# Performance work log

Measured on AMD Instinct MI355X. Metric: run time of the kernel, lower is better.

Reference implementation:

```python
import jax, jax.numpy as jnp
import numpy as np


def setup_inputs() -> dict:
    key = jax.random.key(0)
    k_u, k_wl, k_b, k_c = jax.random.split(key, 4)
    B_, T, D, N = 4, 4096, 1024, 256
    u = jax.random.normal(k_u, (B_, T, D), dtype=jnp.float32)
    # torch init: W_lambda.weight zeros, bias 2.0; B, C xavier_uniform gain=0.5.
    # Use small random weights for W_lambda too so the path is exercised.
    Wl = jax.random.normal(k_wl, (N, D), dtype=jnp.float32) * 0.02
    bl = jnp.full((N,), 2.0, dtype=jnp.float32)
    xav_b = 0.5 * np.sqrt(6.0 / (D + N))
    Wb = jax.random.uniform(k_b, (N, D), dtype=jnp.float32, minval=-xav_b, maxval=xav_b)
    xav_c = 0.5 * np.sqrt(6.0 / (N + D))
    Wc = jax.random.uniform(k_c, (D, N), dtype=jnp.float32, minval=-xav_c, maxval=xav_c)
    Dp = jnp.zeros((D,), dtype=jnp.float32)
    return {"u": u, "Wl": Wl, "bl": bl, "Wb": Wb, "Wc": Wc, "Dp": Dp}


def reference(u, Wl, bl, Wb, Wc, Dp):
    # u: (B, T, D). Precompute per-step gates and inputs with batched GEMMs,
    # then run the diagonal linear recurrence with lax.scan over time.
    lam = jax.nn.sigmoid(jnp.einsum('btd,nd->btn', u, Wl) + bl)  # (B, T, N)
    Bu = jnp.einsum('btd,nd->btn', u, Wb)                         # (B, T, N)

    def step(h, inp):
        lam_t, bu_t = inp            # each (B, N)
        h = lam_t * h + bu_t
        return h, h

    h0 = jnp.zeros((u.shape[0], Wl.shape[0]), dtype=u.dtype)
    # scan over time: move T to leading axis
    _, H = jax.lax.scan(step, h0, (jnp.swapaxes(lam, 0, 1), jnp.swapaxes(Bu, 0, 1)))
    H = jnp.swapaxes(H, 0, 1)        # (B, T, N)
    y = jnp.einsum('btn,dn->btd', H, Wc) + u * Dp
    return y
```

## Files before the change

kernel.cpp:

```cpp
#include <hip/hip_runtime.h>


typedef __bf16 bf16_t;
typedef __attribute__((ext_vector_type(8))) __bf16 bf16x8;
typedef __attribute__((ext_vector_type(4))) __bf16 bf16x4;
typedef __attribute__((ext_vector_type(4))) float f32x4;

#define B_  4
#define T_  4096
#define D_  1024
#define N_  256
#define BT  (B_ * T_)
#define NCHUNK 64
#define CHLEN  (T_ / NCHUNK)

#define GLOAD_LDS16(g, l) __builtin_amdgcn_global_load_lds(              \
    (__attribute__((address_space(1))) void*)(g),                        \
    (__attribute__((address_space(3))) void*)(l), 16, 0, 0)

__global__ void cvt_f32_bf16(const float* __restrict__ in,
                             bf16_t* __restrict__ out, int n4) {
  int i = blockIdx.x * 256 + threadIdx.x;
  if (i >= n4) return;
  float4 v = ((const float4*)in)[i];
  bf16x4 o = {(__bf16)v.x, (__bf16)v.y, (__bf16)v.z, (__bf16)v.w};
  ((bf16x4*)out)[i] = o;
}

__global__ void cvt_wcomb(const float* __restrict__ Wl,
                          const float* __restrict__ Wb,
                          bf16_t* __restrict__ out) {
  int i = blockIdx.x * 256 + threadIdx.x;
  int e = i * 4;
  int j = e >> 10;
  int d = e & 1023;
  const float* src = (j < 256) ? (Wl + (size_t)j * D_ + d)
                               : (Wb + (size_t)(j - 256) * D_ + d);
  float4 v = *(const float4*)src;
  bf16x4 o = {(__bf16)v.x, (__bf16)v.y, (__bf16)v.z, (__bf16)v.w};
  ((bf16x4*)out)[i] = o;
}

__device__ __forceinline__ void mfma_tile(const bf16_t* bufA, const bf16_t* bufB,
                                          int wr, int wc, int r16, int kq,
                                          f32x4 (&acc)[4][4]) {
#pragma unroll
  for (int kk = 0; kk < 2; ++kk) {
    bf16x8 af[4], bfr[4];
#pragma unroll
    for (int m = 0; m < 4; ++m)
      af[m] = *(const bf16x8*)&bufA[(wr * 64 + m * 16 + r16) * 64 + kk * 32 + kq * 8];
#pragma unroll
    for (int n = 0; n < 4; ++n)
      bfr[n] = *(const bf16x8*)&bufB[(wc * 64 + n * 16 + r16) * 64 + kk * 32 + kq * 8];
#pragma unroll
    for (int m = 0; m < 4; ++m)
#pragma unroll
      for (int n = 0; n < 4; ++n)
        acc[m][n] = __builtin_amdgcn_mfma_f32_16x16x32_bf16(af[m], bfr[n], acc[m][n], 0, 0, 0);
  }
}

__global__ __launch_bounds__(256)
void gemm1_kernel(const float* __restrict__ A, const bf16_t* __restrict__ Bm,
                  float* __restrict__ C, const float* __restrict__ bl) {
  __shared__ bf16_t lA[2][128 * 64];
  __shared__ bf16_t lB[2][128 * 64];
  const int wid  = threadIdx.x >> 6;
  const int lane = threadIdx.x & 63;
  const int work = (blockIdx.x & 7) * 64 + (blockIdx.x >> 3);
  const int brow = work >> 2;
  const int bcol = work & 3;
  const int r16 = lane & 15;
  const int kq  = lane >> 4;
  const int wr = wid >> 1, wc = wid & 1;

  f32x4 acc[4][4] = {};

  const int ar = lane >> 4;
  const int ac = (lane & 15) * 4;
  const float* gA = A + (size_t)(brow * 128 + wid * 32 + ar) * D_ + ac;
  bf16_t* lAw[2] = {&lA[0][(wid * 32 + ar) * 64 + ac],
                    &lA[1][(wid * 32 + ar) * 64 + ac]};

  const bf16_t* gB = Bm + (size_t)(bcol * 128 + wid * 8 + (lane >> 3)) * D_ + (lane & 7) * 8;

  {
    float4 va[8];
#pragma unroll
    for (int i = 0; i < 8; ++i)
      va[i] = *(const float4*)(gA + (size_t)(i * 4) * D_);
#pragma unroll
    for (int i = 0; i < 4; ++i)
      GLOAD_LDS16(gB + (size_t)(i * 32) * D_, &lB[0][(wid * 8 + i * 32) * 64]);
#pragma unroll
    for (int i = 0; i < 8; ++i) {
      bf16x4 o = {(__bf16)va[i].x, (__bf16)va[i].y,
                  (__bf16)va[i].z, (__bf16)va[i].w};
      *(bf16x4*)(lAw[0] + i * 4 * 64) = o;
    }
    __syncthreads();
  }

  int cur = 0;
#pragma unroll 1
  for (int k0 = 0; k0 < D_ - 64; k0 += 64) {
    float4 va[8];
#pragma unroll
    for (int i = 0; i < 8; ++i)
      va[i] = *(const float4*)(gA + (size_t)(i * 4) * D_ + k0 + 64);
#pragma unroll
    for (int i = 0; i < 4; ++i)
      GLOAD_LDS16(gB + (size_t)(i * 32) * D_ + k0 + 64,
                  &lB[cur ^ 1][(wid * 8 + i * 32) * 64]);
    mfma_tile(lA[cur], lB[cur], wr, wc, r16, kq, acc);
#pragma unroll
    for (int i = 0; i < 8; ++i) {
      bf16x4 o = {(__bf16)va[i].x, (__bf16)va[i].y,
                  (__bf16)va[i].z, (__bf16)va[i].w};
      *(bf16x4*)(lAw[cur ^ 1] + i * 4 * 64) = o;
    }
    __syncthreads();
    cur ^= 1;
  }
  mfma_tile(lA[cur], lB[cur], wr, wc, r16, kq, acc);

#pragma unroll
  for (int m = 0; m < 4; ++m) {
#pragma unroll
    for (int n = 0; n < 4; ++n) {
      int row0 = brow * 128 + wr * 64 + m * 16 + kq * 4;
      int col  = bcol * 128 + wc * 64 + n * 16 + r16;
#pragma unroll
      for (int j = 0; j < 4; ++j) {
        float v = acc[m][n][j];
        int row = row0 + j;
        if (col < 256) v = 1.0f / (1.0f + __expf(-(v + bl[col])));
        C[(size_t)row * 512 + col] = v;
      }
    }
  }
}

__global__ __launch_bounds__(256)
void gemm2_kernel(const bf16_t* __restrict__ A, const bf16_t* __restrict__ Bm,
                  float* __restrict__ C,
                  const float* __restrict__ u, const float* __restrict__ Dp) {
  __shared__ bf16_t lA[2][128 * 64];
  __shared__ bf16_t lB[2][128 * 64];
  const int wid  = threadIdx.x >> 6;
  const int lane = threadIdx.x & 63;
  const int brow = blockIdx.x;
  const int bcol = blockIdx.y;
  const int r16 = lane & 15;
  const int kq  = lane >> 4;
  const int wr = wid >> 1, wc = wid & 1;

  f32x4 acc[4][4] = {};

  const bf16_t* gA = A + (size_t)(brow * 128 + wid * 8 + (lane >> 3)) * N_ + (lane & 7) * 8;
  const bf16_t* gB = Bm + (size_t)(bcol * 128 + wid * 8 + (lane >> 3)) * N_ + (lane & 7) * 8;

  {
#pragma unroll
    for (int i = 0; i < 4; ++i) {
      GLOAD_LDS16(gA + (size_t)(i * 32) * N_, &lA[0][(wid * 8 + i * 32) * 64]);
      GLOAD_LDS16(gB + (size_t)(i * 32) * N_, &lB[0][(wid * 8 + i * 32) * 64]);
    }
    __syncthreads();
  }
  int cur = 0;
#pragma unroll 1
  for (int k0 = 0; k0 < N_ - 64; k0 += 64) {
#pragma unroll
    for (int i = 0; i < 4; ++i) {
      GLOAD_LDS16(gA + (size_t)(i * 32) * N_ + k0 + 64,
                  &lA[cur ^ 1][(wid * 8 + i * 32) * 64]);
      GLOAD_LDS16(gB + (size_t)(i * 32) * N_ + k0 + 64,
                  &lB[cur ^ 1][(wid * 8 + i * 32) * 64]);
    }
    mfma_tile(lA[cur], lB[cur], wr, wc, r16, kq, acc);
    __syncthreads();
    cur ^= 1;
  }
  mfma_tile(lA[cur], lB[cur], wr, wc, r16, kq, acc);

#pragma unroll
  for (int m = 0; m < 4; ++m) {
#pragma unroll
    for (int n = 0; n < 4; ++n) {
      int row0 = brow * 128 + wr * 64 + m * 16 + kq * 4;
      int col  = bcol * 128 + wc * 64 + n * 16 + r16;
#pragma unroll
      for (int j = 0; j < 4; ++j) {
        int row = row0 + j;
        float v = acc[m][n][j] + Dp[col] * u[(size_t)row * D_ + col];
        C[(size_t)row * D_ + col] = v;
      }
    }
  }
}

__global__ void scan_phase1(const float* __restrict__ Z,
                            float* __restrict__ wsA, float* __restrict__ wsB) {
  int tid = blockIdx.x * 256 + threadIdx.x;
  int n = tid & 255;
  int chunk = (tid >> 8) & (NCHUNK - 1);
  int b = tid >> 14;
  const float* zl = Z + ((size_t)(b * T_ + chunk * CHLEN)) * 512 + n;
  float A = 1.f, h = 0.f;
#pragma unroll 8
  for (int t = 0; t < CHLEN; ++t) {
    float lam = zl[0];
    float bu  = zl[256];
    A *= lam;
    h = fmaf(lam, h, bu);
    zl += 512;
  }
  wsA[tid] = A;
  wsB[tid] = h;
}

__global__ void scan_phase2(const float* __restrict__ wsA,
                            const float* __restrict__ wsB,
                            float* __restrict__ carry) {
  int tid = blockIdx.x * 256 + threadIdx.x;
  int n = tid & 255;
  int b = tid >> 8;
  float h = 0.f;
#pragma unroll
  for (int c = 0; c < NCHUNK; ++c) {
    int idx = (b * NCHUNK + c) * 256 + n;
    carry[idx] = h;
    h = fmaf(wsA[idx], h, wsB[idx]);
  }
}

__global__ void scan_phase3(const float* __restrict__ Z,
                            const float* __restrict__ carry,
                            bf16_t* __restrict__ H) {
  int tid = blockIdx.x * 256 + threadIdx.x;
  int n = tid & 255;
  int chunk = (tid >> 8) & (NCHUNK - 1);
  int b = tid >> 14;
  const float* zl = Z + ((size_t)(b * T_ + chunk * CHLEN)) * 512 + n;
  bf16_t* ho = H + ((size_t)(b * T_ + chunk * CHLEN)) * 256 + n;
  float h = carry[tid];
#pragma unroll 8
  for (int t = 0; t < CHLEN; ++t) {
    float lam = zl[0];
    float bu  = zl[256];
    h = fmaf(lam, h, bu);
    *ho = (__bf16)h;
    zl += 512;
    ho += 256;
  }
}

extern "C" void kernel_launch(void* const* d_in, const int* in_sizes, int n_in,
                              void* d_out, int out_size, void* d_ws, size_t ws_size,
                              hipStream_t stream) {
  const float* u  = (const float*)d_in[0];
  const float* Wl = (const float*)d_in[1];
  const float* bl = (const float*)d_in[2];
  const float* Wb = (const float*)d_in[3];
  const float* Wc = (const float*)d_in[4];
  const float* Dp = (const float*)d_in[5];
  float* y = (float*)d_out;

  char* ws = (char*)d_ws;
  float*  Z     = (float*)(ws + 0);
  bf16_t* H     = (bf16_t*)(ws + 33554432);
  bf16_t* Wcomb = (bf16_t*)(ws + 41943040);
  bf16_t* Wc_bf = (bf16_t*)(ws + 42991616);
  float*  wsA   = (float*)(ws + 43515904);
  float*  wsB   = (float*)(ws + 43778048);
  float*  carry = (float*)(ws + 44040192);

  cvt_wcomb<<<(512 * D_ / 4) / 256, 256, 0, stream>>>(Wl, Wb, Wcomb);
  cvt_f32_bf16<<<(D_ * N_ / 4) / 256, 256, 0, stream>>>(Wc, Wc_bf, D_ * N_ / 4);

  gemm1_kernel<<<512, 256, 0, stream>>>(u, Wcomb, Z, bl);

  scan_phase1<<<(B_ * NCHUNK * N_) / 256, 256, 0, stream>>>(Z, wsA, wsB);
  scan_phase2<<<(B_ * N_) / 256, 256, 0, stream>>>(wsA, wsB, carry);
  scan_phase3<<<(B_ * NCHUNK * N_) / 256, 256, 0, stream>>>(Z, carry, H);

  dim3 g2(BT / 128, D_ / 128);
  gemm2_kernel<<<g2, 256, 0, stream>>>(H, Wc_bf, y, u, Dp);
}
```

Measured before the change: 210.8 us.

## Use 8 waves per GEMM block and XOR-swizzle LDS tiles

Both GEMM kernels move from 4 to 8 waves per 128x128 block, so each wave computes a 64x32 sub-tile with half the accumulators. The loaders are rewritten to match, and an XOR swizzle is applied to LDS writes and reads to avoid bank conflicts on the bf16x8 fragment loads. The aim is more latency hiding per CU and fewer LDS conflicts. In exchange, each wave reuses fewer fragments per MFMA and the swizzle adds index arithmetic.

```diff
diff --git a/kernel.cpp b/kernel.cpp
--- a/kernel.cpp
+++ b/kernel.cpp
@@ -41,27 +41,32 @@
   ((bf16x4*)out)[i] = o;
 }
 
-__device__ __forceinline__ void mfma_tile(const bf16_t* bufA, const bf16_t* bufB,
-                                          int wr, int wc, int r16, int kq,
-                                          f32x4 (&acc)[4][4]) {
+__device__ __forceinline__ void mfma_tile8(const bf16_t* bufA, const bf16_t* bufB,
+                                           int wr, int wc, int r16, int kq,
+                                           f32x4 (&acc)[4][2]) {
+  const int sw = (r16 & 7) << 3;
 #pragma unroll
   for (int kk = 0; kk < 2; ++kk) {
-    bf16x8 af[4], bfr[4];
+    bf16x8 af[4], bfr[2];
+#pragma unroll
+    for (int m = 0; m < 4; ++m) {
+      int idx = (wr * 64 + m * 16 + r16) * 64 + kk * 32 + kq * 8;
+      af[m] = *(const bf16x8*)&bufA[idx ^ sw];
+    }
+#pragma unroll
+    for (int n = 0; n < 2; ++n) {
+      int idx = (wc * 32 + n * 16 + r16) * 64 + kk * 32 + kq * 8;
+      bfr[n] = *(const bf16x8*)&bufB[idx ^ sw];
+    }
 #pragma unroll
     for (int m = 0; m < 4; ++m)
-      af[m] = *(const bf16x8*)&bufA[(wr * 64 + m * 16 + r16) * 64 + kk * 32 + kq * 8];
-#pragma unroll
-    for (int n = 0; n < 4; ++n)
-      bfr[n] = *(const bf16x8*)&bufB[(wc * 64 + n * 16 + r16) * 64 + kk * 32 + kq * 8];
-#pragma unroll
-    for (int m = 0; m < 4; ++m)
-#pragma unroll
-      for (int n = 0; n < 4; ++n)
+#pragma unroll
+      for (int n = 0; n < 2; ++n)
         acc[m][n] = __builtin_amdgcn_mfma_f32_16x16x32_bf16(af[m], bfr[n], acc[m][n], 0, 0, 0);
   }
 }
 
-__global__ __launch_bounds__(256)
+__global__ __launch_bounds__(512, 4)
 void gemm1_kernel(const float* __restrict__ A, const bf16_t* __restrict__ Bm,
                   float* __restrict__ C, const float* __restrict__ bl) {
   __shared__ bf16_t lA[2][128 * 64];
@@ -73,31 +78,32 @@
   const int bcol = work & 3;
   const int r16 = lane & 15;
   const int kq  = lane >> 4;
-  const int wr = wid >> 1, wc = wid & 1;
-
-  f32x4 acc[4][4] = {};
+  const int wr = wid >> 2, wc = wid & 3;
+
+  f32x4 acc[4][2] = {};
 
   const int ar = lane >> 4;
   const int ac = (lane & 15) * 4;
-  const float* gA = A + (size_t)(brow * 128 + wid * 32 + ar) * D_ + ac;
-  bf16_t* lAw[2] = {&lA[0][(wid * 32 + ar) * 64 + ac],
-                    &lA[1][(wid * 32 + ar) * 64 + ac]};
-
-  const bf16_t* gB = Bm + (size_t)(bcol * 128 + wid * 8 + (lane >> 3)) * D_ + (lane & 7) * 8;
+  const float* gA = A + (size_t)(brow * 128 + wid * 16 + ar) * D_ + ac;
+  const int aw_base = (wid * 16 + ar) * 64 + ac;
+
+  const bf16_t* gB = Bm + (size_t)(bcol * 128 + wid * 16 + (lane >> 3)) * D_
+                        + (size_t)(((lane & 7) ^ (lane >> 3)) * 8);
 
   {
-    float4 va[8];
-#pragma unroll
-    for (int i = 0; i < 8; ++i)
+    float4 va[4];
+#pragma unroll
+    for (int i = 0; i < 4; ++i)
       va[i] = *(const float4*)(gA + (size_t)(i * 4) * D_);
 #pragma unroll
-    for (int i = 0; i < 4; ++i)
-      GLOAD_LDS16(gB + (size_t)(i * 32) * D_, &lB[0][(wid * 8 + i * 32) * 64]);
-#pragma unroll
-    for (int i = 0; i < 8; ++i) {
+    for (int i = 0; i < 2; ++i)
+      GLOAD_LDS16(gB + (size_t)(i * 8) * D_, &lB[0][(wid * 16 + i * 8) * 64]);
+#pragma unroll
+    for (int i = 0; i < 4; ++i) {
       bf16x4 o = {(__bf16)va[i].x, (__bf16)va[i].y,
                   (__bf16)va[i].z, (__bf16)va[i].w};
-      *(bf16x4*)(lAw[0] + i * 4 * 64) = o;
+      int idx = (aw_base + i * 4 * 64) ^ (((ar + 4 * (i & 1)) & 7) << 3);
+      *(bf16x4*)&lA[0][idx] = o;
     }
     __syncthreads();
   }
@@ -105,32 +111,33 @@
   int cur = 0;
 #pragma unroll 1
   for (int k0 = 0; k0 < D_ - 64; k0 += 64) {
-    float4 va[8];
-#pragma unroll
-    for (int i = 0; i < 8; ++i)
+    float4 va[4];
+#pragma unroll
+    for (int i = 0; i < 4; ++i)
       va[i] = *(const float4*)(gA + (size_t)(i * 4) * D_ + k0 + 64);
 #pragma unroll
-    for (int i = 0; i < 4; ++i)
-      GLOAD_LDS16(gB + (size_t)(i * 32) * D_ + k0 + 64,
-                  &lB[cur ^ 1][(wid * 8 + i * 32) * 64]);
-    mfma_tile(lA[cur], lB[cur], wr, wc, r16, kq, acc);
-#pragma unroll
-    for (int i = 0; i < 8; ++i) {
+    for (int i = 0; i < 2; ++i)
+      GLOAD_LDS16(gB + (size_t)(i * 8) * D_ + k0 + 64,
+                  &lB[cur ^ 1][(wid * 16 + i * 8) * 64]);
+    mfma_tile8(lA[cur], lB[cur], wr, wc, r16, kq, acc);
+#pragma unroll
+    for (int i = 0; i < 4; ++i) {
       bf16x4 o = {(__bf16)va[i].x, (__bf16)va[i].y,
                   (__bf16)va[i].z, (__bf16)va[i].w};
-      *(bf16x4*)(lAw[cur ^ 1] + i * 4 * 64) = o;
+      int idx = (aw_base + i * 4 * 64) ^ (((ar + 4 * (i & 1)) & 7) << 3);
+      *(bf16x4*)&lA[cur ^ 1][idx] = o;
     }
     __syncthreads();
     cur ^= 1;
   }
-  mfma_tile(lA[cur], lB[cur], wr, wc, r16, kq, acc);
+  mfma_tile8(lA[cur], lB[cur], wr, wc, r16, kq, acc);
 
 #pragma unroll
   for (int m = 0; m < 4; ++m) {
 #pragma unroll
-    for (int n = 0; n < 4; ++n) {
+    for (int n = 0; n < 2; ++n) {
       int row0 = brow * 128 + wr * 64 + m * 16 + kq * 4;
-      int col  = bcol * 128 + wc * 64 + n * 16 + r16;
+      int col  = bcol * 128 + wc * 32 + n * 16 + r16;
 #pragma unroll
       for (int j = 0; j < 4; ++j) {
         float v = acc[m][n][j];
@@ -142,7 +149,7 @@
   }
 }
 
-__global__ __launch_bounds__(256)
+__global__ __launch_bounds__(512, 4)
 void gemm2_kernel(const bf16_t* __restrict__ A, const bf16_t* __restrict__ Bm,
                   float* __restrict__ C,
                   const float* __restrict__ u, const float* __restrict__ Dp) {
@@ -154,18 +161,19 @@
   const int bcol = blockIdx.y;
   const int r16 = lane & 15;
   const int kq  = lane >> 4;
-  const int wr = wid >> 1, wc = wid & 1;
-
-  f32x4 acc[4][4] = {};
-
-  const bf16_t* gA = A + (size_t)(brow * 128 + wid * 8 + (lane >> 3)) * N_ + (lane & 7) * 8;
-  const bf16_t* gB = Bm + (size_t)(bcol * 128 + wid * 8 + (lane >> 3)) * N_ + (lane & 7) * 8;
+  const int wr = wid >> 2, wc = wid & 3;
+
+  f32x4 acc[4][2] = {};
+
+  const size_t scol = ((lane & 7) ^ (lane >> 3)) * 8;
+  const bf16_t* gA = A + (size_t)(brow * 128 + wid * 16 + (lane >> 3)) * N_ + scol;
+  const bf16_t* gB = Bm + (size_t)(bcol * 128 + wid * 16 + (lane >> 3)) * N_ + scol;
 
   {
 #pragma unroll
-    for (int i = 0; i < 4; ++i) {
-      GLOAD_LDS16(gA + (size_t)(i * 32) * N_, &lA[0][(wid * 8 + i * 32) * 64]);
-      GLOAD_LDS16(gB + (size_t)(i * 32) * N_, &lB[0][(wid * 8 + i * 32) * 64]);
+    for (int i = 0; i < 2; ++i) {
+      GLOAD_LDS16(gA + (size_t)(i * 8) * N_, &lA[0][(wid * 16 + i * 8) * 64]);
+      GLOAD_LDS16(gB + (size_t)(i * 8) * N_, &lB[0][(wid * 16 + i * 8) * 64]);
     }
     __syncthreads();
   }
@@ -173,24 +181,24 @@
 #pragma unroll 1
   for (int k0 = 0; k0 < N_ - 64; k0 += 64) {
 #pragma unroll
-    for (int i = 0; i < 4; ++i) {
-      GLOAD_LDS16(gA + (size_t)(i * 32) * N_ + k0 + 64,
-                  &lA[cur ^ 1][(wid * 8 + i * 32) * 64]);
-      GLOAD_LDS16(gB + (size_t)(i * 32) * N_ + k0 + 64,
-                  &lB[cur ^ 1][(wid * 8 + i * 32) * 64]);
-    }
-    mfma_tile(lA[cur], lB[cur], wr, wc, r16, kq, acc);
+    for (int i = 0; i < 2; ++i) {
+      GLOAD_LDS16(gA + (size_t)(i * 8) * N_ + k0 + 64,
+                  &lA[cur ^ 1][(wid * 16 + i * 8) * 64]);
+      GLOAD_LDS16(gB + (size_t)(i * 8) * N_ + k0 + 64,
+                  &lB[cur ^ 1][(wid * 16 + i * 8) * 64]);
+    }
+    mfma_tile8(lA[cur], lB[cur], wr, wc, r16, kq, acc);
     __syncthreads();
     cur ^= 1;
   }
-  mfma_tile(lA[cur], lB[cur], wr, wc, r16, kq, acc);
+  mfma_tile8(lA[cur], lB[cur], wr, wc, r16, kq, acc);
 
 #pragma unroll
   for (int m = 0; m < 4; ++m) {
 #pragma unroll
-    for (int n = 0; n < 4; ++n) {
+    for (int n = 0; n < 2; ++n) {
       int row0 = brow * 128 + wr * 64 + m * 16 + kq * 4;
-      int col  = bcol * 128 + wc * 64 + n * 16 + r16;
+      int col  = bcol * 128 + wc * 32 + n * 16 + r16;
 #pragma unroll
       for (int j = 0; j < 4; ++j) {
         int row = row0 + j;
@@ -280,12 +288,12 @@
   cvt_wcomb<<<(512 * D_ / 4) / 256, 256, 0, stream>>>(Wl, Wb, Wcomb);
   cvt_f32_bf16<<<(D_ * N_ / 4) / 256, 256, 0, stream>>>(Wc, Wc_bf, D_ * N_ / 4);
 
-  gemm1_kernel<<<512, 256, 0, stream>>>(u, Wcomb, Z, bl);
+  gemm1_kernel<<<512, 512, 0, stream>>>(u, Wcomb, Z, bl);
 
   scan_phase1<<<(B_ * NCHUNK * N_) / 256, 256, 0, stream>>>(Z, wsA, wsB);
   scan_phase2<<<(B_ * N_) / 256, 256, 0, stream>>>(wsA, wsB, carry);
   scan_phase3<<<(B_ * NCHUNK * N_) / 256, 256, 0, stream>>>(Z, carry, H);
 
   dim3 g2(BT / 128, D_ / 128);
-  gemm2_kernel<<<g2, 256, 0, stream>>>(H, Wc_bf, y, u, Dp);
-}
+  gemm2_kernel<<<g2, 512, 0, stream>>>(H, Wc_bf, y, u, Dp);
+}
```

Result: faster. 200.6 us (-4.8%).
